# Optimization experiments

Measured on AMD Instinct MI355X. Metric: run time of the kernel, lower is better.

## Reference

```python
import jax, jax.numpy as jnp
import numpy as np

HEADS = 20


def cape_embed(f, P):
    # f: [b, s, d], P: [b, s, 4, 4]; rotate channel groups of 4 by P
    b, s, d = f.shape
    f4 = f.reshape(b, s, d // 4, 4)
    out = jnp.einsum('bsik,bskj->bsij', f4, P)
    return out.reshape(b, s, d)


def setup_inputs() -> dict:
    key = jax.random.key(0)
    ks = jax.random.split(key, 9)
    bt, l, d = 2, 1024, 1280  # (b*t_out, tokens, channels)
    t_out, b = 2, 1
    sd = 1.0 / np.sqrt(d)
    return {
        'hidden_states': jax.random.normal(ks[0], (bt, l, d), jnp.float32),
        'p_out': jax.random.normal(ks[1], (b, t_out, 4, 4), jnp.float32) * 0.5,
        'p_out_inv': jax.random.normal(ks[2], (b, t_out, 4, 4), jnp.float32) * 0.5,
        'Wq': jax.random.normal(ks[3], (d, d), jnp.float32) * sd,
        'Wk': jax.random.normal(ks[4], (d, d), jnp.float32) * sd,
        'Wv': jax.random.normal(ks[5], (d, d), jnp.float32) * sd,
        'Wo': jax.random.normal(ks[6], (d, d), jnp.float32) * sd,
        'bo': jnp.zeros((d,), jnp.float32),
    }


def reference(hidden_states, p_out, p_out_inv, Wq, Wk, Wv, Wo, bo):
    residual = hidden_states  # [(b t_out), l, d]
    b = p_out.shape[0]
    t_out = p_out.shape[1]
    bt, l, d = hidden_states.shape
    s = t_out * l
    hd = d // HEADS
    scale = hd ** -0.5

    # rearrange '(b t_out) l d -> b (t_out l) d'
    hs = hidden_states.reshape(b, s, d)

    q = hs @ Wq
    k = hs @ Wk
    v = hs @ Wv

    # repeat per-frame CAPE matrices over spatial tokens: 'b t f g -> b (t l) f g'
    Pq = jnp.repeat(p_out_inv, l, axis=1)  # [b, s, 4, 4]
    Pk = jnp.repeat(p_out, l, axis=1)      # self-attn: p_in := p_out
    q = cape_embed(q, Pq)
    k = cape_embed(k, Pk)

    # head split: [b, s, d] -> [b, h, s, hd]
    qh = q.reshape(b, s, HEADS, hd).transpose(0, 2, 1, 3)
    kh = k.reshape(b, s, HEADS, hd).transpose(0, 2, 1, 3)
    vh = v.reshape(b, s, HEADS, hd).transpose(0, 2, 1, 3)

    scores = jnp.einsum('bhsd,bhtd->bhst', qh, kh) * scale
    probs = jax.nn.softmax(scores, axis=-1)
    out = jnp.einsum('bhst,bhtd->bhsd', probs, vh)

    out = out.transpose(0, 2, 1, 3).reshape(b, s, d)
    out = out @ Wo + bo

    # rearrange 'b (t_out l) d -> (b t_out) l d'
    out = out.reshape(bt, l, d)
    out = out + residual  # residual_connection; rescale_output_factor = 1.0
    return out
```

## Files before the change

kernel.cpp:

```cpp
#include <hip/hip_runtime.h>

typedef short short8 __attribute__((ext_vector_type(8)));
typedef short short4v __attribute__((ext_vector_type(4)));
typedef float f32x4 __attribute__((ext_vector_type(4)));
typedef __bf16 bf16x8 __attribute__((ext_vector_type(8)));
typedef _Float16 half4 __attribute__((ext_vector_type(4)));

__device__ __forceinline__ short f2bf(float x) {
  unsigned u = __builtin_bit_cast(unsigned, x);
  u += 0x7fffu + ((u >> 16) & 1u);
  return (short)(u >> 16);
}

__device__ __forceinline__ f32x4 mfma16(short8 a, short8 b, f32x4 c) {
  return __builtin_amdgcn_mfma_f32_16x16x32_bf16(
      __builtin_bit_cast(bf16x8, a), __builtin_bit_cast(bf16x8, b), c, 0, 0, 0);
}

__device__ __forceinline__ void async16(void* lds, const void* g) {
  __builtin_amdgcn_global_load_lds(
      (const __attribute__((address_space(1))) unsigned*)g,
      (__attribute__((address_space(3))) unsigned*)lds, 16, 0, 0);
}


__global__ __launch_bounds__(256) void cvt_bf16_kernel(
    const float* __restrict__ x, short* __restrict__ y, int n) {
  int i = blockIdx.x * 256 + threadIdx.x;
  if (i < n) y[i] = f2bf(x[i]);
}

__global__ __launch_bounds__(256) void capeT_kernel(
    const float* __restrict__ W, const float* __restrict__ P, float scale,
    short* __restrict__ dst0, short* __restrict__ dst1) {
  __shared__ float tile[32][33];
  const int ND = 1280, KD = 1280;
  int bn = blockIdx.x * 32, bk = blockIdx.y * 32;
  int tx = threadIdx.x, ty = threadIdx.y;
  for (int i = ty; i < 32; i += 8)
    tile[i][tx] = W[(size_t)(bk + i) * ND + bn + tx];
  __syncthreads();
  for (int c = ty; c < 32; c += 8) {
    float v0, v1;
    if (P) {
      int g = c & ~3, jj = c & 3;
      float a0 = 0.f, a1 = 0.f;
#pragma unroll
      for (int j = 0; j < 4; j++) {
        float wv = tile[tx][g + j];
        a0 += wv * P[j * 4 + jj];
        a1 += wv * P[16 + j * 4 + jj];
      }
      v0 = a0 * scale;
      v1 = a1 * scale;
    } else {
      v0 = v1 = tile[tx][c] * scale;
    }
    size_t o = (size_t)(bn + c) * KD + bk + tx;
    dst0[o] = f2bf(v0);
    if (dst1) dst1[o] = f2bf(v1);
  }
}


template <int EPI>
__global__ __launch_bounds__(256) void gemm128_kernel(
    const short* __restrict__ A, const short* __restrict__ B0,
    const short* __restrict__ B1, int M, int N, int K,
    const float* __restrict__ bias, const float* __restrict__ resid,
    float* __restrict__ out, short* __restrict__ qb,
    short* __restrict__ ktl, _Float16* __restrict__ vtl) {
  __shared__ __align__(16) short As[2][128][32];
  __shared__ __align__(16) short Bs[2][128][32];
  int tid = threadIdx.x;
  int l = tid & 63, w = tid >> 6;
  int wr = w >> 1, wc = w & 1;
  int lr = l & 15, lg = l >> 4;
  int bm = blockIdx.y * 128, bn = blockIdx.x * 128;
  const short* BT = (bm >= 1024) ? B1 : B0;
  f32x4 acc[4][4] = {};

  auto stage = [&](int b, int k0) {
    const short* ga = A + (size_t)(bm + (tid >> 2)) * K + k0 + (tid & 3) * 8;
    const short* gb = BT + (size_t)(bn + (tid >> 2)) * K + k0 + (tid & 3) * 8;
    char* la = (char*)&As[b][0][0] + w * 1024;
    char* lb = (char*)&Bs[b][0][0] + w * 1024;
    async16(la, ga);
    async16(la + 4096, ga + (size_t)64 * K);
    async16(lb, gb);
    async16(lb + 4096, gb + (size_t)64 * K);
  };

  auto compute = [&](int b) {
    const short* Ab = &As[b][0][0];
    const short* Bb = &Bs[b][0][0];
    short8 af[4], bf_[4];
#pragma unroll
    for (int mi = 0; mi < 4; mi++)
      af[mi] = *(const short8*)(Ab + (wr * 64 + mi * 16 + lr) * 32 + lg * 8);
#pragma unroll
    for (int nj = 0; nj < 4; nj++)
      bf_[nj] = *(const short8*)(Bb + (wc * 64 + nj * 16 + lr) * 32 + lg * 8);
#pragma unroll
    for (int mi = 0; mi < 4; mi++)
#pragma unroll
      for (int nj = 0; nj < 4; nj++)
        acc[mi][nj] = mfma16(af[mi], bf_[nj], acc[mi][nj]);
  };

  int nk = K >> 5;
  stage(0, 0);
  for (int ks = 0; ks < nk; ks += 2) {
    __syncthreads();
    if (ks + 1 < nk) stage(1, (ks + 1) << 5);
    compute(0);
    __syncthreads();
    if (ks + 2 < nk) stage(0, (ks + 2) << 5);
    compute(1);
  }

#pragma unroll
  for (int mi = 0; mi < 4; mi++)
#pragma unroll
    for (int nj = 0; nj < 4; nj++)
#pragma unroll
      for (int i = 0; i < 4; i++) {
        int row = bm + wr * 64 + mi * 16 + lg * 4 + i;
        int col = bn + wc * 64 + nj * 16 + lr;
        float v = acc[mi][nj][i];
        if (EPI == 1) {
          out[(size_t)row * N + col] = v + bias[col] + resid[(size_t)row * N + col];
        } else {
          int s = row;
          if (col < 1280) {
            qb[(((size_t)(col >> 6)) * 2048 + s) * 64 + (col & 63)] = f2bf(v);
          } else if (col < 2560) {
            int cc = col - 1280;
            int h = cc >> 6, d = cc & 63;
            int kt = s >> 6, r = s & 63;
            int kcol = (((d >> 3) ^ (r & 7)) << 3) | (d & 7);
            ktl[(((size_t)h * 32 + kt) * 64 + r) * 64 + kcol] = f2bf(v);
          } else {
            int cc = col - 2560;
            int h = cc >> 6, dv = cc & 63;
            int kt = s >> 6, kk = s & 63;
            int vcol = (((kk >> 2) ^ (dv & 15)) << 2) | (kk & 3);
            vtl[(((size_t)h * 32 + kt) * 64 + dv) * 64 + vcol] = (_Float16)v;
          }
        }
      }
}

__global__ __launch_bounds__(256) void attn_kernel(
    const short* __restrict__ qb, const short* __restrict__ k_tiled,
    const _Float16* __restrict__ v_tiled, short* __restrict__ attn_out) {
  const int S = 2048, HD = 64;
  int h = blockIdx.x;
  int qblk = blockIdx.y;
  int tid = threadIdx.x;
  int w = tid >> 6, l = tid & 63;
  int lr = l & 15, lg = l >> 4;
  int q0 = qblk * 64 + w * 16;

  __shared__ __align__(16) short Kl[2][64][64];
  __shared__ __align__(16) _Float16 Vl[2][64][64];

  const short* qptr = qb + ((size_t)h * S + q0 + lr) * HD;
  short8 qf0 = *(const short8*)(qptr + lg * 8);
  short8 qf1 = *(const short8*)(qptr + 32 + lg * 8);

  auto stageKV = [&](int b, int kt) {
    const short* gk = k_tiled + (((size_t)h * 32 + kt) << 12) + tid * 8;
    const _Float16* gv = v_tiled + (((size_t)h * 32 + kt) << 12) + tid * 8;
    char* lk = (char*)&Kl[b][0][0] + w * 1024;
    char* lv = (char*)&Vl[b][0][0] + w * 1024;
    async16(lk, gk);
    async16(lk + 4096, gk + 2048);
    async16(lv, gv);
    async16(lv + 4096, gv + 2048);
  };

  float m = -1e30f, lsum = 0.f;
  f32x4 oacc[4] = {};

  auto compute_tile = [&](int buf) {
    const short* Kb = &Kl[buf][0][0];
    const _Float16* Vb = &Vl[buf][0][0];
    f32x4 st[4];
#pragma unroll
    for (int kk = 0; kk < 4; kk++) {
      int r = kk * 16 + lr;
      int sw = r & 7;
      short8 kf0 = *(const short8*)(Kb + r * 64 + ((lg ^ sw) << 3));
      short8 kf1 = *(const short8*)(Kb + r * 64 + (((4 + lg) ^ sw) << 3));
      f32x4 s0 = {};
      s0 = mfma16(kf0, qf0, s0);
      s0 = mfma16(kf1, qf1, s0);
      st[kk] = s0;
    }
    float m0 = fmaxf(fmaxf(st[0][0], st[0][1]), fmaxf(st[0][2], st[0][3]));
    float m1 = fmaxf(fmaxf(st[1][0], st[1][1]), fmaxf(st[1][2], st[1][3]));
    float m2 = fmaxf(fmaxf(st[2][0], st[2][1]), fmaxf(st[2][2], st[2][3]));
    float m3 = fmaxf(fmaxf(st[3][0], st[3][1]), fmaxf(st[3][2], st[3][3]));
    float tm = fmaxf(fmaxf(m0, m1), fmaxf(m2, m3));
    tm = fmaxf(tm, __shfl_xor(tm, 16));
    tm = fmaxf(tm, __shfl_xor(tm, 32));
    if (!__all(tm <= m + 8.0f)) {
      float mnew = fmaxf(m, tm);
      float fac = __builtin_amdgcn_exp2f(m - mnew);
      lsum *= fac;
#pragma unroll
      for (int i = 0; i < 4; i++) {
        float fi = __shfl(fac, lg * 4 + i);
#pragma unroll
        for (int nb = 0; nb < 4; nb++) oacc[nb][i] *= fi;
      }
      m = mnew;
    }
    half4 pf[4];
    float ps[4];
#pragma unroll
    for (int kk = 0; kk < 4; kk++) {
      float p0 = __builtin_amdgcn_exp2f(st[kk][0] - m);
      float p1 = __builtin_amdgcn_exp2f(st[kk][1] - m);
      float p2 = __builtin_amdgcn_exp2f(st[kk][2] - m);
      float p3 = __builtin_amdgcn_exp2f(st[kk][3] - m);
      pf[kk][0] = (_Float16)p0;
      pf[kk][1] = (_Float16)p1;
      pf[kk][2] = (_Float16)p2;
      pf[kk][3] = (_Float16)p3;
      ps[kk] = (p0 + p1) + (p2 + p3);
    }
    float psum = (ps[0] + ps[1]) + (ps[2] + ps[3]);
    psum += __shfl_xor(psum, 16);
    psum += __shfl_xor(psum, 32);
    lsum += psum;
#pragma unroll
    for (int kk = 0; kk < 4; kk++) {
      half4 vf[4];
#pragma unroll
      for (int nb = 0; nb < 4; nb++) {
        int dv = nb * 16 + lr;
        vf[nb] = *(const half4*)(Vb + dv * 64 + ((((kk << 2) + lg) ^ lr) << 2));
      }
#pragma unroll
      for (int nb = 0; nb < 4; nb++)
        oacc[nb] = __builtin_amdgcn_mfma_f32_16x16x16f16(pf[kk], vf[nb], oacc[nb], 0, 0, 0);
    }
  };

  stageKV(0, 0);
  for (int kt2 = 0; kt2 < 32; kt2 += 2) {
    __syncthreads();
    if (kt2 + 1 < 32) stageKV(1, kt2 + 1);
    compute_tile(0);
    __syncthreads();
    if (kt2 + 2 < 32) stageKV(0, kt2 + 2);
    compute_tile(1);
  }

#pragma unroll
  for (int i = 0; i < 4; i++) {
    float li = __shfl(lsum, lg * 4 + i);
    float inv = 1.0f / li;
    int row = q0 + lg * 4 + i;
#pragma unroll
    for (int nb = 0; nb < 4; nb++)
      attn_out[(size_t)row * 1280 + h * 64 + nb * 16 + lr] = f2bf(oacc[nb][i] * inv);
  }
}


extern "C" void kernel_launch(void* const* d_in, const int* in_sizes, int n_in,
                              void* d_out, int out_size, void* d_ws, size_t ws_size,
                              hipStream_t stream) {
  const float* hs = (const float*)d_in[0];
  const float* p_out = (const float*)d_in[1];
  const float* p_inv = (const float*)d_in[2];
  const float* Wq = (const float*)d_in[3];
  const float* Wk = (const float*)d_in[4];
  const float* Wv = (const float*)d_in[5];
  const float* Wo = (const float*)d_in[6];
  const float* bo = (const float*)d_in[7];
  float* out = (float*)d_out;
  char* ws = (char*)d_ws;

  short* hs_bf = (short*)(ws + 0);
  short* BT0 = (short*)(ws + 5242880);
  short* BT1 = (short*)(ws + 15073280);
  short* wo_t = (short*)(ws + 24903680);
  short* q_bf = (short*)(ws + 28180480);
  short* k_tiled = (short*)(ws + 33423360);
  _Float16* v_tiled = (_Float16*)(ws + 38666240);
  short* attn_bf = (short*)(ws + 43909120);

  const float QSCALE = 0.125f * 1.44269504f;
  const int n_hs = 2048 * 1280;
  cvt_bf16_kernel<<<(n_hs + 255) / 256, 256, 0, stream>>>(hs, hs_bf, n_hs);

  dim3 tb(32, 8), tg(40, 40);
  capeT_kernel<<<tg, tb, 0, stream>>>(Wq, p_inv, QSCALE, BT0, BT1);
  capeT_kernel<<<tg, tb, 0, stream>>>(Wk, p_out, 1.0f,
                                      BT0 + (size_t)1280 * 1280, BT1 + (size_t)1280 * 1280);
  capeT_kernel<<<tg, tb, 0, stream>>>(Wv, nullptr, 1.0f,
                                      BT0 + (size_t)2560 * 1280, BT1 + (size_t)2560 * 1280);
  capeT_kernel<<<tg, tb, 0, stream>>>(Wo, nullptr, 1.0f, wo_t, nullptr);

  gemm128_kernel<2><<<dim3(30, 16), 256, 0, stream>>>(
      hs_bf, BT0, BT1, 2048, 3840, 1280,
      nullptr, nullptr, nullptr, q_bf, k_tiled, v_tiled);

  attn_kernel<<<dim3(20, 32), 256, 0, stream>>>(q_bf, k_tiled, v_tiled, attn_bf);

  gemm128_kernel<1><<<dim3(10, 16), 256, 0, stream>>>(
      attn_bf, wo_t, wo_t, 2048, 1280, 1280,
      bo, hs, out, nullptr, nullptr, nullptr);
}
```

Before: 141.3 us.

## Merge weight-prep launches, shrink attention and output-GEMM tiles, add MFMA priority hints

Folds the four weight transpose/CAPE launches into one 3D-grid launch to cut launch overhead. Halves the attention block to 128 threads (32 queries per block), doubling grid size to 1280 blocks for better CU fill. The blocks still stage the full 64-row K/V tiles, so each block now has 2 waves doing all the loads. Replaces the 128x128 output GEMM with a 64x64-tile kernel to go from 160 to 640 blocks. Also adds s_setprio around the MFMA sections and packed fp16 conversion for the probabilities. The smaller tiles raise K/V and operand reload traffic per unit of work.

```diff
diff --git a/kernel.cpp b/kernel.cpp
--- a/kernel.cpp
+++ b/kernel.cpp
@@ -5,6 +5,7 @@
 typedef float f32x4 __attribute__((ext_vector_type(4)));
 typedef __bf16 bf16x8 __attribute__((ext_vector_type(8)));
 typedef _Float16 half4 __attribute__((ext_vector_type(4)));
+typedef _Float16 half2v __attribute__((ext_vector_type(2)));
 
 __device__ __forceinline__ short f2bf(float x) {
   unsigned u = __builtin_bit_cast(unsigned, x);
@@ -30,11 +31,25 @@
   if (i < n) y[i] = f2bf(x[i]);
 }
 
-__global__ __launch_bounds__(256) void capeT_kernel(
-    const float* __restrict__ W, const float* __restrict__ P, float scale,
-    short* __restrict__ dst0, short* __restrict__ dst1) {
+__global__ __launch_bounds__(256) void capeT_all_kernel(
+    const float* __restrict__ Wq, const float* __restrict__ Wk,
+    const float* __restrict__ Wv, const float* __restrict__ Wo,
+    const float* __restrict__ p_inv, const float* __restrict__ p_out,
+    float qscale, short* __restrict__ BT0, short* __restrict__ BT1,
+    short* __restrict__ wo_t) {
+  const int ND = 1280, KD = 1280;
+  const size_t SEC = (size_t)1280 * 1280;
+  int z = blockIdx.z;
+  const float* W;
+  const float* P;
+  float scale = 1.0f;
+  short *d0, *d1;
+  if (z == 0) { W = Wq; P = p_inv; scale = qscale; d0 = BT0; d1 = BT1; }
+  else if (z == 1) { W = Wk; P = p_out; d0 = BT0 + SEC; d1 = BT1 + SEC; }
+  else if (z == 2) { W = Wv; P = nullptr; d0 = BT0 + 2 * SEC; d1 = BT1 + 2 * SEC; }
+  else { W = Wo; P = nullptr; d0 = wo_t; d1 = nullptr; }
+
   __shared__ float tile[32][33];
-  const int ND = 1280, KD = 1280;
   int bn = blockIdx.x * 32, bk = blockIdx.y * 32;
   int tx = threadIdx.x, ty = threadIdx.y;
   for (int i = ty; i < 32; i += 8)
@@ -57,19 +72,17 @@
       v0 = v1 = tile[tx][c] * scale;
     }
     size_t o = (size_t)(bn + c) * KD + bk + tx;
-    dst0[o] = f2bf(v0);
-    if (dst1) dst1[o] = f2bf(v1);
-  }
-}
-
-
-template <int EPI>
-__global__ __launch_bounds__(256) void gemm128_kernel(
+    d0[o] = f2bf(v0);
+    if (d1) d1[o] = f2bf(v1);
+  }
+}
+
+
+__global__ __launch_bounds__(256) void gemm128_qkv_kernel(
     const short* __restrict__ A, const short* __restrict__ B0,
     const short* __restrict__ B1, int M, int N, int K,
-    const float* __restrict__ bias, const float* __restrict__ resid,
-    float* __restrict__ out, short* __restrict__ qb,
-    short* __restrict__ ktl, _Float16* __restrict__ vtl) {
+    short* __restrict__ qb, short* __restrict__ ktl,
+    _Float16* __restrict__ vtl) {
   __shared__ __align__(16) short As[2][128][32];
   __shared__ __align__(16) short Bs[2][128][32];
   int tid = threadIdx.x;
@@ -128,30 +141,88 @@
         int row = bm + wr * 64 + mi * 16 + lg * 4 + i;
         int col = bn + wc * 64 + nj * 16 + lr;
         float v = acc[mi][nj][i];
-        if (EPI == 1) {
-          out[(size_t)row * N + col] = v + bias[col] + resid[(size_t)row * N + col];
+        int s = row;
+        if (col < 1280) {
+          qb[(((size_t)(col >> 6)) * 2048 + s) * 64 + (col & 63)] = f2bf(v);
+        } else if (col < 2560) {
+          int cc = col - 1280;
+          int h = cc >> 6, d = cc & 63;
+          int kt = s >> 6, r = s & 63;
+          int kcol = (((d >> 3) ^ (r & 7)) << 3) | (d & 7);
+          ktl[(((size_t)h * 32 + kt) * 64 + r) * 64 + kcol] = f2bf(v);
         } else {
-          int s = row;
-          if (col < 1280) {
-            qb[(((size_t)(col >> 6)) * 2048 + s) * 64 + (col & 63)] = f2bf(v);
-          } else if (col < 2560) {
-            int cc = col - 1280;
-            int h = cc >> 6, d = cc & 63;
-            int kt = s >> 6, r = s & 63;
-            int kcol = (((d >> 3) ^ (r & 7)) << 3) | (d & 7);
-            ktl[(((size_t)h * 32 + kt) * 64 + r) * 64 + kcol] = f2bf(v);
-          } else {
-            int cc = col - 2560;
-            int h = cc >> 6, dv = cc & 63;
-            int kt = s >> 6, kk = s & 63;
-            int vcol = (((kk >> 2) ^ (dv & 15)) << 2) | (kk & 3);
-            vtl[(((size_t)h * 32 + kt) * 64 + dv) * 64 + vcol] = (_Float16)v;
-          }
+          int cc = col - 2560;
+          int h = cc >> 6, dv = cc & 63;
+          int kt = s >> 6, kk = s & 63;
+          int vcol = (((kk >> 2) ^ (dv & 15)) << 2) | (kk & 3);
+          vtl[(((size_t)h * 32 + kt) * 64 + dv) * 64 + vcol] = (_Float16)v;
         }
       }
 }
 
-__global__ __launch_bounds__(256) void attn_kernel(
+
+__global__ __launch_bounds__(256) void gemm64_o_kernel(
+    const short* __restrict__ A, const short* __restrict__ BT,
+    int M, int N, int K, const float* __restrict__ bias,
+    const float* __restrict__ resid, float* __restrict__ out) {
+  __shared__ __align__(16) short As[2][64][32];
+  __shared__ __align__(16) short Bs[2][64][32];
+  int tid = threadIdx.x;
+  int l = tid & 63, w = tid >> 6;
+  int wr = w >> 1, wc = w & 1;
+  int lr = l & 15, lg = l >> 4;
+  int bm = blockIdx.y * 64, bn = blockIdx.x * 64;
+  f32x4 acc[2][2] = {};
+
+  auto stage = [&](int b, int k0) {
+    const short* ga = A + (size_t)(bm + (tid >> 2)) * K + k0 + (tid & 3) * 8;
+    const short* gb = BT + (size_t)(bn + (tid >> 2)) * K + k0 + (tid & 3) * 8;
+    async16((char*)&As[b][0][0] + w * 1024, ga);
+    async16((char*)&Bs[b][0][0] + w * 1024, gb);
+  };
+
+  auto compute = [&](int b) {
+    const short* Ab = &As[b][0][0];
+    const short* Bb = &Bs[b][0][0];
+    short8 af[2], bf_[2];
+#pragma unroll
+    for (int mi = 0; mi < 2; mi++)
+      af[mi] = *(const short8*)(Ab + (wr * 32 + mi * 16 + lr) * 32 + lg * 8);
+#pragma unroll
+    for (int nj = 0; nj < 2; nj++)
+      bf_[nj] = *(const short8*)(Bb + (wc * 32 + nj * 16 + lr) * 32 + lg * 8);
+#pragma unroll
+    for (int mi = 0; mi < 2; mi++)
+#pragma unroll
+      for (int nj = 0; nj < 2; nj++)
+        acc[mi][nj] = mfma16(af[mi], bf_[nj], acc[mi][nj]);
+  };
+
+  int nk = K >> 5;
+  stage(0, 0);
+  for (int ks = 0; ks < nk; ks += 2) {
+    __syncthreads();
+    if (ks + 1 < nk) stage(1, (ks + 1) << 5);
+    compute(0);
+    __syncthreads();
+    if (ks + 2 < nk) stage(0, (ks + 2) << 5);
+    compute(1);
+  }
+
+#pragma unroll
+  for (int mi = 0; mi < 2; mi++)
+#pragma unroll
+    for (int nj = 0; nj < 2; nj++)
+#pragma unroll
+      for (int i = 0; i < 4; i++) {
+        int row = bm + wr * 32 + mi * 16 + lg * 4 + i;
+        int col = bn + wc * 32 + nj * 16 + lr;
+        out[(size_t)row * N + col] =
+            acc[mi][nj][i] + bias[col] + resid[(size_t)row * N + col];
+      }
+}
+
+__global__ __launch_bounds__(128) void attn_kernel(
     const short* __restrict__ qb, const short* __restrict__ k_tiled,
     const _Float16* __restrict__ v_tiled, short* __restrict__ attn_out) {
   const int S = 2048, HD = 64;
@@ -160,7 +231,7 @@
   int tid = threadIdx.x;
   int w = tid >> 6, l = tid & 63;
   int lr = l & 15, lg = l >> 4;
-  int q0 = qblk * 64 + w * 16;
+  int q0 = qblk * 32 + w * 16;
 
   __shared__ __align__(16) short Kl[2][64][64];
   __shared__ __align__(16) _Float16 Vl[2][64][64];
@@ -174,10 +245,11 @@
     const _Float16* gv = v_tiled + (((size_t)h * 32 + kt) << 12) + tid * 8;
     char* lk = (char*)&Kl[b][0][0] + w * 1024;
     char* lv = (char*)&Vl[b][0][0] + w * 1024;
-    async16(lk, gk);
-    async16(lk + 4096, gk + 2048);
-    async16(lv, gv);
-    async16(lv + 4096, gv + 2048);
+#pragma unroll
+    for (int r = 0; r < 4; r++) {
+      async16(lk + r * 2048, gk + r * 1024);
+      async16(lv + r * 2048, gv + r * 1024);
+    }
   };
 
   float m = -1e30f, lsum = 0.f;
@@ -187,6 +259,7 @@
     const short* Kb = &Kl[buf][0][0];
     const _Float16* Vb = &Vl[buf][0][0];
     f32x4 st[4];
+    __builtin_amdgcn_s_setprio(1);
 #pragma unroll
     for (int kk = 0; kk < 4; kk++) {
       int r = kk * 16 + lr;
@@ -198,6 +271,7 @@
       s0 = mfma16(kf1, qf1, s0);
       st[kk] = s0;
     }
+    __builtin_amdgcn_s_setprio(0);
     float m0 = fmaxf(fmaxf(st[0][0], st[0][1]), fmaxf(st[0][2], st[0][3]));
     float m1 = fmaxf(fmaxf(st[1][0], st[1][1]), fmaxf(st[1][2], st[1][3]));
     float m2 = fmaxf(fmaxf(st[2][0], st[2][1]), fmaxf(st[2][2], st[2][3]));
@@ -225,10 +299,10 @@
       float p1 = __builtin_amdgcn_exp2f(st[kk][1] - m);
       float p2 = __builtin_amdgcn_exp2f(st[kk][2] - m);
       float p3 = __builtin_amdgcn_exp2f(st[kk][3] - m);
-      pf[kk][0] = (_Float16)p0;
-      pf[kk][1] = (_Float16)p1;
-      pf[kk][2] = (_Float16)p2;
-      pf[kk][3] = (_Float16)p3;
+      half2v lo = __builtin_bit_cast(half2v, __builtin_amdgcn_cvt_pkrtz(p0, p1));
+      half2v hi = __builtin_bit_cast(half2v, __builtin_amdgcn_cvt_pkrtz(p2, p3));
+      pf[kk][0] = lo[0]; pf[kk][1] = lo[1];
+      pf[kk][2] = hi[0]; pf[kk][3] = hi[1];
       ps[kk] = (p0 + p1) + (p2 + p3);
     }
     float psum = (ps[0] + ps[1]) + (ps[2] + ps[3]);
@@ -243,9 +317,11 @@
         int dv = nb * 16 + lr;
         vf[nb] = *(const half4*)(Vb + dv * 64 + ((((kk << 2) + lg) ^ lr) << 2));
       }
+      __builtin_amdgcn_s_setprio(1);
 #pragma unroll
       for (int nb = 0; nb < 4; nb++)
         oacc[nb] = __builtin_amdgcn_mfma_f32_16x16x16f16(pf[kk], vf[nb], oacc[nb], 0, 0, 0);
+      __builtin_amdgcn_s_setprio(0);
     }
   };
 
@@ -298,21 +374,14 @@
   const int n_hs = 2048 * 1280;
   cvt_bf16_kernel<<<(n_hs + 255) / 256, 256, 0, stream>>>(hs, hs_bf, n_hs);
 
-  dim3 tb(32, 8), tg(40, 40);
-  capeT_kernel<<<tg, tb, 0, stream>>>(Wq, p_inv, QSCALE, BT0, BT1);
-  capeT_kernel<<<tg, tb, 0, stream>>>(Wk, p_out, 1.0f,
-                                      BT0 + (size_t)1280 * 1280, BT1 + (size_t)1280 * 1280);
-  capeT_kernel<<<tg, tb, 0, stream>>>(Wv, nullptr, 1.0f,
-                                      BT0 + (size_t)2560 * 1280, BT1 + (size_t)2560 * 1280);
-  capeT_kernel<<<tg, tb, 0, stream>>>(Wo, nullptr, 1.0f, wo_t, nullptr);
-
-  gemm128_kernel<2><<<dim3(30, 16), 256, 0, stream>>>(
-      hs_bf, BT0, BT1, 2048, 3840, 1280,
-      nullptr, nullptr, nullptr, q_bf, k_tiled, v_tiled);
-
-  attn_kernel<<<dim3(20, 32), 256, 0, stream>>>(q_bf, k_tiled, v_tiled, attn_bf);
-
-  gemm128_kernel<1><<<dim3(10, 16), 256, 0, stream>>>(
-      attn_bf, wo_t, wo_t, 2048, 1280, 1280,
-      bo, hs, out, nullptr, nullptr, nullptr);
-}
+  capeT_all_kernel<<<dim3(40, 40, 4), dim3(32, 8), 0, stream>>>(
+      Wq, Wk, Wv, Wo, p_inv, p_out, QSCALE, BT0, BT1, wo_t);
+
+  gemm128_qkv_kernel<<<dim3(30, 16), 256, 0, stream>>>(
+      hs_bf, BT0, BT1, 2048, 3840, 1280, q_bf, k_tiled, v_tiled);
+
+  attn_kernel<<<dim3(20, 64), 128, 0, stream>>>(q_bf, k_tiled, v_tiled, attn_bf);
+
+  gemm64_o_kernel<<<dim3(20, 32), 256, 0, stream>>>(
+      attn_bf, wo_t, 2048, 1280, 1280, bo, hs, out);
+}
```

Result: slower. 158.1 us (+11.9%).
